# Kernel optimization log

Hardware: AMD Instinct MI355X
Metric: run time of the kernel (lower is better)

## Reference

```python
import jax, jax.numpy as jnp
import numpy as np


def conv2d(x, w, b, stride, pad):
    out = jax.lax.conv_general_dilated(
        x, w, (stride, stride), [(pad, pad), (pad, pad)],
        dimension_numbers=("NCHW", "OIHW", "NCHW"))
    return out + b[None, :, None, None]


def setup_inputs() -> dict:
    key = jax.random.key(0)
    ks = jax.random.split(key, 7)
    B, Cin, Cout = 4, 32, 64
    x = jax.random.normal(ks[0], (B, Cin, 256, 256), jnp.float32)
    prev_h = jax.random.normal(ks[1], (B, Cout, 320, 320), jnp.float32)
    prev_c = jax.random.normal(ks[2], (B, Cout, 320, 320), jnp.float32)
    Wc = jax.random.normal(ks[3], (Cout, Cin, 5, 5), jnp.float32) * 0.05
    bc = jax.random.normal(ks[4], (Cout,), jnp.float32) * 0.05
    Wg = jax.random.normal(ks[5], (4 * Cout, 2 * Cout, 3, 3), jnp.float32) * 0.05
    bg = jax.random.normal(ks[6], (4 * Cout,), jnp.float32) * 0.05
    return {"x": x, "prev_h": prev_h, "prev_c": prev_c,
            "Wc": Wc, "bc": bc, "Wg": Wg, "bg": bg,
            "ey": 64, "ex": 64, "eh": 256, "ew": 256}


def reference(x, prev_h, prev_c, Wc, bc, Wg, bg, ey, ex, eh, ew):
    # axis_scale = 1; state indices are event coords // 2
    ey2, ex2, eh2, ew2 = ey // 2, ex // 2, eh // 2, ew // 2
    pad = 1  # ConvLSTM kernel_size // 2 (external padding)

    # ConvLayer: stride-2 conv + ReLU
    x_conv = jax.nn.relu(conv2d(x, Wc, bc, stride=2, pad=2))  # [B,Cout,eh2,ew2]

    def crop_with_padding(arr):
        H, W = arr.shape[-2], arr.shape[-1]
        y0, y1 = max(0, ey2 - pad), min(H, ey2 + eh2 + pad)
        x0, x1 = max(0, ex2 - pad), min(W, ex2 + ew2 + pad)
        c = arr[..., y0:y1, x0:x1]
        pt, pl = max(0, pad - ey2), max(0, pad - ex2)
        pb, pr = max(0, ey2 + eh2 + pad - H), max(0, ex2 + ew2 + pad - W)
        if pt or pl or pb or pr:
            c = jnp.pad(c, ((0, 0), (0, 0), (pt, pb), (pl, pr)))
        return c

    h_crop = crop_with_padding(prev_h)  # [B,Cout,eh2+2,ew2+2]
    c_crop = crop_with_padding(prev_c)

    x_pad = jnp.pad(x_conv, ((0, 0), (0, 0), (pad, pad), (pad, pad)))
    stacked = jnp.concatenate([x_pad, h_crop], axis=1)  # [B,2*Cout,eh2+2,ew2+2]
    gates = conv2d(stacked, Wg, bg, stride=1, pad=0)    # [B,4*Cout,eh2,ew2]
    i_g, r_g, o_g, c_g = jnp.split(gates, 4, axis=1)

    prev_cell = c_crop[..., pad:-pad, pad:-pad]
    cell = jax.nn.sigmoid(r_g) * prev_cell + jax.nn.sigmoid(i_g) * jnp.tanh(c_g)
    hidden = jax.nn.sigmoid(o_g) * jnp.tanh(cell)

    new_h = prev_h.at[..., ey2:ey2 + eh2, ex2:ex2 + ew2].set(hidden)
    new_c = prev_c.at[..., ey2:ey2 + eh2, ex2:ex2 + ew2].set(cell)
    return (hidden, new_h, new_c)
```

## Files before the change

kernel.cpp:

```cpp
#include <hip/hip_runtime.h>
#include <math.h>


#define OFF_NEWH 4194304
#define OFF_NEWC 30408704
#define S_ELEMS  8652800
#define XP_OFF   8652800
#define WP_OFF   17305600
#define WP1_OFF  17600512

typedef __attribute__((ext_vector_type(8))) short bf16x8;
typedef __attribute__((ext_vector_type(4))) float f32x4;

__device__ __forceinline__ float sigm(float v) { return 1.0f / (1.0f + expf(-v)); }

__device__ __forceinline__ unsigned short f2bf(float f) {
    unsigned u = __builtin_bit_cast(unsigned, f);
    u = (u + 0x7FFFu + ((u >> 16) & 1u)) >> 16;
    return (unsigned short)u;
}
__device__ __forceinline__ unsigned pack2(float lo, float hi) {
    return (unsigned)f2bf(lo) | ((unsigned)f2bf(hi) << 16);
}

__global__ __launch_bounds__(256) void pack_wc(
    const float* __restrict__ Wc, unsigned short* __restrict__ Wp1)
{
    int i = blockIdx.x * 256 + threadIdx.x;
    if (i < 51200) {
        int tap = i >> 11;
        int rem = i & 2047;
        int co  = rem >> 5;
        int ci  = rem & 31;
        Wp1[i] = f2bf(Wc[(co * 32 + ci) * 25 + tap]);
    }
}

__global__ __launch_bounds__(256) void pack_wg(
    const float* __restrict__ Wg, unsigned short* __restrict__ Wp)
{
    int i = blockIdx.x * 256 + threadIdx.x;
    if (i < 294912) {
        int tap = i >> 15;
        int rem = i & 32767;
        int co  = rem >> 7;
        int ci  = rem & 127;
        Wp[i] = f2bf(Wg[(co * 128 + ci) * 9 + tap]);
    }
}

__global__ __launch_bounds__(256) void xpose_x(
    const float* __restrict__ x, unsigned short* __restrict__ Xp)
{
    __shared__ __align__(16) float lds[32 * 260];
    const int y = blockIdx.x, n = blockIdx.y, tid = threadIdx.x;

    for (int u = tid; u < 2048; u += 256) {
        int c = u >> 6, x4 = (u & 63) << 2;
        float4 v = *(const float4*)(x + (((n * 32 + c) * 256 + y) << 8) + x4);
        *(float4*)(&lds[c * 260 + x4]) = v;
    }
    __syncthreads();

    const int px = tid;
    unsigned short* dst = Xp + (((n * 260) + (y + 2)) * 260 + (px + 2)) * 32;
#pragma unroll
    for (int q = 0; q < 4; ++q) {
        uint4 w;
        w.x = pack2(lds[(q * 8 + 0) * 260 + px], lds[(q * 8 + 1) * 260 + px]);
        w.y = pack2(lds[(q * 8 + 2) * 260 + px], lds[(q * 8 + 3) * 260 + px]);
        w.z = pack2(lds[(q * 8 + 4) * 260 + px], lds[(q * 8 + 5) * 260 + px]);
        w.w = pack2(lds[(q * 8 + 6) * 260 + px], lds[(q * 8 + 7) * 260 + px]);
        *(uint4*)(dst + q * 8) = w;
    }
}

__global__ __launch_bounds__(256) void hconv(
    const float* __restrict__ prev_h, unsigned short* __restrict__ S)
{
    const int sy = blockIdx.x, n = blockIdx.y, tid = threadIdx.x;
    for (int u = tid; u < 1040; u += 256) {
        int px = u >> 3, ch = u & 7;
        const float* src = prev_h + (((n * 64 + ch * 8) * 320 + (31 + sy)) * 320) + 31 + px;
        uint4 w;
        w.x = pack2(src[0 * 102400], src[1 * 102400]);
        w.y = pack2(src[2 * 102400], src[3 * 102400]);
        w.z = pack2(src[4 * 102400], src[5 * 102400]);
        w.w = pack2(src[6 * 102400], src[7 * 102400]);
        *(uint4*)(S + (((n * 130 + sy) * 130 + px) << 7) + 64 + ch * 8) = w;
    }
}

__global__ __launch_bounds__(256) void conv1_mfma(
    const unsigned short* __restrict__ Xp,
    const unsigned short* __restrict__ Wp1,
    const float* __restrict__ bc,
    unsigned short* __restrict__ S)
{
    __shared__ __align__(16) unsigned short patch[361 * 40];

    const int tid  = threadIdx.x;
    const int lane = tid & 63;
    const int wv   = tid >> 6;
    const int l15  = lane & 15;
    const int g    = lane >> 4;

    const int tile = blockIdx.x;
    const int ty0  = (tile >> 4) << 3;
    const int tx0  = (tile & 15) << 3;
    const int n    = blockIdx.y;

    for (int u = tid; u < 1444; u += 256) {
        int pos = u >> 2, ch = u & 3;
        int iyl = pos / 19, ixl = pos - iyl * 19;
        const unsigned short* src =
            Xp + (((n * 260) + 2 * ty0 + iyl) * 260 + 2 * tx0 + ixl) * 32 + ch * 8;
        *(bf16x8*)(&patch[pos * 40 + ch * 8]) = *(const bf16x8*)src;
    }
    __syncthreads();

    f32x4 acc[4];
#pragma unroll
    for (int cf = 0; cf < 4; ++cf)
#pragma unroll
        for (int e = 0; e < 4; ++e) acc[cf][e] = 0.f;

    const unsigned short* Abase = Wp1 + (wv * 16 + l15) * 32 + g * 8;
    const int posBase = (2 * (l15 >> 3)) * 19 + 2 * (l15 & 7);
    const unsigned short* Bbase = patch + posBase * 40 + g * 8;

#pragma unroll
    for (int tap = 0; tap < 25; ++tap) {
        const int ky = tap / 5, kx = tap % 5;
        bf16x8 a = *(const bf16x8*)(Abase + tap * 2048);
        const unsigned short* Bt = Bbase + (ky * 19 + kx) * 40;
#pragma unroll
        for (int cf = 0; cf < 4; ++cf) {
            bf16x8 b = *(const bf16x8*)(Bt + cf * (76 * 40));
            acc[cf] = __builtin_amdgcn_mfma_f32_16x16x32_bf16(a, b, acc[cf], 0, 0, 0);
        }
    }

#pragma unroll
    for (int cf = 0; cf < 4; ++cf) {
        int p  = cf * 16 + l15;
        int oh = ty0 + (p >> 3);
        int ow = tx0 + (p & 7);
        int co = wv * 16 + g * 4;
        float v0 = fmaxf(acc[cf][0] + bc[co + 0], 0.f);
        float v1 = fmaxf(acc[cf][1] + bc[co + 1], 0.f);
        float v2 = fmaxf(acc[cf][2] + bc[co + 2], 0.f);
        float v3 = fmaxf(acc[cf][3] + bc[co + 3], 0.f);
        uint2 w;
        w.x = pack2(v0, v1);
        w.y = pack2(v2, v3);
        *(uint2*)(S + (((n * 130 + 1 + oh) * 130 + 1 + ow) << 7) + co) = w;
    }
}

__global__ __launch_bounds__(256) void gates_mfma(
    const unsigned short* __restrict__ S,
    const float* __restrict__ prev_c,
    const unsigned short* __restrict__ Wp,
    const float* __restrict__ bg,
    float* __restrict__ out)
{
    __shared__ __align__(16) unsigned short patch[100 * 136];

    const int tid  = threadIdx.x;
    const int lane = tid & 63;
    const int wv   = tid >> 6;
    const int l15  = lane & 15;
    const int g    = lane >> 4;

    const int tile = blockIdx.x;
    const int ty0  = (tile >> 4) << 3;
    const int tx0  = (tile & 15) << 3;
    const int n    = blockIdx.y;

    for (int u = tid; u < 1600; u += 256) {
        int pos = u >> 4, ch = u & 15;
        int y = pos / 10, xx = pos - y * 10;
        const unsigned short* src =
            S + (((n * 130 + ty0 + y) * 130 + tx0 + xx) << 7) + ch * 8;
        *(bf16x8*)(&patch[pos * 136 + ch * 8]) = *(const bf16x8*)src;
    }
    __syncthreads();

    f32x4 acc[4][4];
#pragma unroll
    for (int i = 0; i < 4; ++i)
#pragma unroll
        for (int j = 0; j < 4; ++j)
#pragma unroll
            for (int e = 0; e < 4; ++e) acc[i][j][e] = 0.f;

    const unsigned short* Abase = Wp + (wv * 16 + l15) * 128 + g * 8;
    const int bb = (l15 >> 3) * 10 + (l15 & 7);

    for (int tap = 0; tap < 9; ++tap) {
        const int ky = tap / 3;
        const int kx = tap - ky * 3;
        const int koff = ky * 10 + kx;
        const unsigned short* At = Abase + tap * 32768;
        const unsigned short* Bt = patch + (bb + koff) * 136 + g * 8;
#pragma unroll
        for (int chunk = 0; chunk < 4; ++chunk) {
            bf16x8 a0 = *(const bf16x8*)(At + 0 * 8192 + chunk * 32);
            bf16x8 a1 = *(const bf16x8*)(At + 1 * 8192 + chunk * 32);
            bf16x8 a2 = *(const bf16x8*)(At + 2 * 8192 + chunk * 32);
            bf16x8 a3 = *(const bf16x8*)(At + 3 * 8192 + chunk * 32);
            const unsigned short* pb = Bt + chunk * 32;
            bf16x8 b0 = *(const bf16x8*)(pb + 0 * 2720);
            bf16x8 b1 = *(const bf16x8*)(pb + 1 * 2720);
            bf16x8 b2 = *(const bf16x8*)(pb + 2 * 2720);
            bf16x8 b3 = *(const bf16x8*)(pb + 3 * 2720);
            acc[0][0] = __builtin_amdgcn_mfma_f32_16x16x32_bf16(a0, b0, acc[0][0], 0, 0, 0);
            acc[0][1] = __builtin_amdgcn_mfma_f32_16x16x32_bf16(a0, b1, acc[0][1], 0, 0, 0);
            acc[0][2] = __builtin_amdgcn_mfma_f32_16x16x32_bf16(a0, b2, acc[0][2], 0, 0, 0);
            acc[0][3] = __builtin_amdgcn_mfma_f32_16x16x32_bf16(a0, b3, acc[0][3], 0, 0, 0);
            acc[1][0] = __builtin_amdgcn_mfma_f32_16x16x32_bf16(a1, b0, acc[1][0], 0, 0, 0);
            acc[1][1] = __builtin_amdgcn_mfma_f32_16x16x32_bf16(a1, b1, acc[1][1], 0, 0, 0);
            acc[1][2] = __builtin_amdgcn_mfma_f32_16x16x32_bf16(a1, b2, acc[1][2], 0, 0, 0);
            acc[1][3] = __builtin_amdgcn_mfma_f32_16x16x32_bf16(a1, b3, acc[1][3], 0, 0, 0);
            acc[2][0] = __builtin_amdgcn_mfma_f32_16x16x32_bf16(a2, b0, acc[2][0], 0, 0, 0);
            acc[2][1] = __builtin_amdgcn_mfma_f32_16x16x32_bf16(a2, b1, acc[2][1], 0, 0, 0);
            acc[2][2] = __builtin_amdgcn_mfma_f32_16x16x32_bf16(a2, b2, acc[2][2], 0, 0, 0);
            acc[2][3] = __builtin_amdgcn_mfma_f32_16x16x32_bf16(a2, b3, acc[2][3], 0, 0, 0);
            acc[3][0] = __builtin_amdgcn_mfma_f32_16x16x32_bf16(a3, b0, acc[3][0], 0, 0, 0);
            acc[3][1] = __builtin_amdgcn_mfma_f32_16x16x32_bf16(a3, b1, acc[3][1], 0, 0, 0);
            acc[3][2] = __builtin_amdgcn_mfma_f32_16x16x32_bf16(a3, b2, acc[3][2], 0, 0, 0);
            acc[3][3] = __builtin_amdgcn_mfma_f32_16x16x32_bf16(a3, b3, acc[3][3], 0, 0, 0);
        }
    }

#pragma unroll
    for (int cf = 0; cf < 4; ++cf) {
        int p  = cf * 16 + l15;
        int oh = ty0 + (p >> 3);
        int ow = tx0 + (p & 7);
#pragma unroll
        for (int r = 0; r < 4; ++r) {
            int c = wv * 16 + g * 4 + r;
            float ig = acc[0][cf][r] + bg[c];
            float rg = acc[1][cf][r] + bg[64 + c];
            float og = acc[2][cf][r] + bg[128 + c];
            float gg = acc[3][cf][r] + bg[192 + c];
            float pc = prev_c[((n * 64 + c) * 320 + (32 + oh)) * 320 + (32 + ow)];
            float cell = sigm(rg) * pc + sigm(ig) * tanhf(gg);
            float hid  = sigm(og) * tanhf(cell);
            out[((n * 64 + c) * 128 + oh) * 128 + ow] = hid;
            out[OFF_NEWH + ((n * 64 + c) * 320 + (32 + oh)) * 320 + (32 + ow)] = hid;
            out[OFF_NEWC + ((n * 64 + c) * 320 + (32 + oh)) * 320 + (32 + ow)] = cell;
        }
    }
}

__global__ __launch_bounds__(256) void copy_f4(
    const float4* __restrict__ src, float4* __restrict__ dst, int n4)
{
    int i = blockIdx.x * blockDim.x + threadIdx.x;
    int stride = gridDim.x * blockDim.x;
    for (; i < n4; i += stride) dst[i] = src[i];
}

extern "C" void kernel_launch(void* const* d_in, const int* in_sizes, int n_in,
                              void* d_out, int out_size, void* d_ws, size_t ws_size,
                              hipStream_t stream)
{
    const float* x      = (const float*)d_in[0];
    const float* prev_h = (const float*)d_in[1];
    const float* prev_c = (const float*)d_in[2];
    const float* Wc     = (const float*)d_in[3];
    const float* bc     = (const float*)d_in[4];
    const float* Wg     = (const float*)d_in[5];
    const float* bg     = (const float*)d_in[6];

    float* out = (float*)d_out;
    unsigned short* S   = (unsigned short*)d_ws;
    unsigned short* Xp  = S + XP_OFF - 0;
    unsigned short* Wp  = S + WP_OFF;
    unsigned short* Wp1 = S + WP1_OFF;
    Xp = S + S_ELEMS;

    hipMemsetAsync(S,  0, (size_t)S_ELEMS * 2, stream);
    hipMemsetAsync(Xp, 0, (size_t)S_ELEMS * 2, stream);

    const int n4 = 26214400 / 4;
    copy_f4<<<2048, 256, 0, stream>>>((const float4*)prev_h, (float4*)(out + OFF_NEWH), n4);
    copy_f4<<<2048, 256, 0, stream>>>((const float4*)prev_c, (float4*)(out + OFF_NEWC), n4);

    pack_wg<<<1152, 256, 0, stream>>>(Wg, Wp);
    pack_wc<<<200, 256, 0, stream>>>(Wc, Wp1);
    xpose_x<<<dim3(256, 4), 256, 0, stream>>>(x, Xp);
    hconv<<<dim3(130, 4), 256, 0, stream>>>(prev_h, S);
    conv1_mfma<<<dim3(256, 4), 256, 0, stream>>>(Xp, Wp1, bc, S);
    gates_mfma<<<dim3(256, 4), 256, 0, stream>>>(S, prev_c, Wp, bg, out);
}
```

Before: 621.3 us.

## Pre-swizzle gate weights for coalesced loads and stage hconv through LDS

```diff
diff --git a/kernel.cpp b/kernel.cpp
--- a/kernel.cpp
+++ b/kernel.cpp
@@ -5,7 +5,6 @@
 #define OFF_NEWH 4194304
 #define OFF_NEWC 30408704
 #define S_ELEMS  8652800
-#define XP_OFF   8652800
 #define WP_OFF   17305600
 #define WP1_OFF  17600512
 
@@ -39,13 +38,18 @@
 __global__ __launch_bounds__(256) void pack_wg(
     const float* __restrict__ Wg, unsigned short* __restrict__ Wp)
 {
-    int i = blockIdx.x * 256 + threadIdx.x;
-    if (i < 294912) {
-        int tap = i >> 15;
-        int rem = i & 32767;
-        int co  = rem >> 7;
-        int ci  = rem & 127;
-        Wp[i] = f2bf(Wg[(co * 128 + ci) * 9 + tap]);
+    int idx = blockIdx.x * 256 + threadIdx.x;
+    if (idx < 294912) {
+        int e     = idx & 7;
+        int lane  = (idx >> 3) & 63;
+        int wv2   = (idx >> 9) & 3;
+        int i     = (idx >> 11) & 3;
+        int chunk = (idx >> 13) & 3;
+        int tap   = idx >> 15;
+        int l15 = lane & 15, g = lane >> 4;
+        int co = i * 64 + wv2 * 16 + l15;
+        int ci = chunk * 32 + g * 8 + e;
+        Wp[idx] = f2bf(Wg[(co * 128 + ci) * 9 + tap]);
     }
 }
 
@@ -78,16 +82,33 @@
 __global__ __launch_bounds__(256) void hconv(
     const float* __restrict__ prev_h, unsigned short* __restrict__ S)
 {
+    __shared__ float lds[64 * 132];
     const int sy = blockIdx.x, n = blockIdx.y, tid = threadIdx.x;
-    for (int u = tid; u < 1040; u += 256) {
-        int px = u >> 3, ch = u & 7;
-        const float* src = prev_h + (((n * 64 + ch * 8) * 320 + (31 + sy)) * 320) + 31 + px;
-        uint4 w;
-        w.x = pack2(src[0 * 102400], src[1 * 102400]);
-        w.y = pack2(src[2 * 102400], src[3 * 102400]);
-        w.z = pack2(src[4 * 102400], src[5 * 102400]);
-        w.w = pack2(src[6 * 102400], src[7 * 102400]);
-        *(uint4*)(S + (((n * 130 + sy) * 130 + px) << 7) + 64 + ch * 8) = w;
+    const float* base = prev_h + ((n * 64) * 320 + (31 + sy)) * 320 + 31;
+
+    for (int e = tid; e < 8192; e += 256) {
+        int ch = e >> 7, px = e & 127;
+        lds[ch * 132 + px] = base[ch * 102400 + px];
+    }
+    if (tid < 128) {
+        int ch = tid & 63, px = 128 + (tid >> 6);
+        lds[ch * 132 + px] = base[ch * 102400 + px];
+    }
+    __syncthreads();
+
+    for (int t = tid; t < 260; t += 256) {
+        int px = t >> 1, half = t & 1;
+        unsigned short* dst = S + (((n * 130 + sy) * 130 + px) << 7) + 64 + half * 32;
+#pragma unroll
+        for (int q = 0; q < 4; ++q) {
+            const float* r = &lds[(half * 32 + q * 8) * 132 + px];
+            uint4 w;
+            w.x = pack2(r[0 * 132], r[1 * 132]);
+            w.y = pack2(r[2 * 132], r[3 * 132]);
+            w.z = pack2(r[4 * 132], r[5 * 132]);
+            w.w = pack2(r[6 * 132], r[7 * 132]);
+            *(uint4*)(dst + q * 8) = w;
+        }
     }
 }
 
@@ -195,21 +216,21 @@
 #pragma unroll
             for (int e = 0; e < 4; ++e) acc[i][j][e] = 0.f;
 
-    const unsigned short* Abase = Wp + (wv * 16 + l15) * 128 + g * 8;
+    const bf16x8* WpV = (const bf16x8*)Wp;
     const int bb = (l15 >> 3) * 10 + (l15 & 7);
 
     for (int tap = 0; tap < 9; ++tap) {
         const int ky = tap / 3;
         const int kx = tap - ky * 3;
         const int koff = ky * 10 + kx;
-        const unsigned short* At = Abase + tap * 32768;
         const unsigned short* Bt = patch + (bb + koff) * 136 + g * 8;
 #pragma unroll
         for (int chunk = 0; chunk < 4; ++chunk) {
-            bf16x8 a0 = *(const bf16x8*)(At + 0 * 8192 + chunk * 32);
-            bf16x8 a1 = *(const bf16x8*)(At + 1 * 8192 + chunk * 32);
-            bf16x8 a2 = *(const bf16x8*)(At + 2 * 8192 + chunk * 32);
-            bf16x8 a3 = *(const bf16x8*)(At + 3 * 8192 + chunk * 32);
+            const bf16x8* Av = WpV + (tap * 4 + chunk) * 1024 + tid;
+            bf16x8 a0 = Av[0];
+            bf16x8 a1 = Av[256];
+            bf16x8 a2 = Av[512];
+            bf16x8 a3 = Av[768];
             const unsigned short* pb = Bt + chunk * 32;
             bf16x8 b0 = *(const bf16x8*)(pb + 0 * 2720);
             bf16x8 b1 = *(const bf16x8*)(pb + 1 * 2720);
@@ -278,10 +299,9 @@
 
     float* out = (float*)d_out;
     unsigned short* S   = (unsigned short*)d_ws;
-    unsigned short* Xp  = S + XP_OFF - 0;
+    unsigned short* Xp  = S + S_ELEMS;
     unsigned short* Wp  = S + WP_OFF;
     unsigned short* Wp1 = S + WP1_OFF;
-    Xp = S + S_ELEMS;
 
     hipMemsetAsync(S,  0, (size_t)S_ELEMS * 2, stream);
     hipMemsetAsync(Xp, 0, (size_t)S_ELEMS * 2, stream);
```

Measured after the change: 556.0 us. -10.5%, faster.
